# Kernel tuning notes

Measured on AMD Instinct MI355X. Metric: run time of the kernel, lower is better.

## Reference

```python
import jax, jax.numpy as jnp
import numpy as np

N_NODES = 50000
N_EDGES = 200000
N_GRAPH = 1024
H = 128          # hidden_channels
POS = 48         # pos_offset
NF = 256         # num_filters in SchNetInteraction
L = 5            # n_layers
NFF = 512
MAX_ITEM = 300


def ssp(v):
    # shifted softplus used by SchNet
    return jax.nn.softplus(v) - jnp.log(2.0)


def setup_inputs() -> dict:
    key = jax.random.key(0)
    ks = iter(jax.random.split(key, 40))
    s = 0.05
    inp = {}
    inp['x'] = jax.random.randint(next(ks), (N_NODES,), 0, MAX_ITEM)
    inp['edge_index'] = jax.random.randint(next(ks), (2, N_EDGES), 0, N_NODES)
    inp['edge_attr'] = jax.random.normal(next(ks), (N_EDGES, 4), jnp.float32)
    inp['batch'] = jnp.sort(jax.random.randint(next(ks), (N_NODES,), 0, N_GRAPH))
    inp['pos'] = jax.random.normal(next(ks), (N_NODES, 3), jnp.float32)
    # embedding / projection params
    vert = jax.random.normal(next(ks), (MAX_ITEM + 1, H - POS), jnp.float32) * s
    inp['vert_emb'] = vert.at[MAX_ITEM].set(0.0)  # padding_idx
    inp['pos_w'] = jax.random.normal(next(ks), (POS, 3), jnp.float32) * s
    inp['edge_w'] = jax.random.normal(next(ks), (H, 4), jnp.float32) * s
    # per-layer SchNetInteraction params (stacked over L)
    inp['filt_w1'] = jax.random.normal(next(ks), (L, NF, H), jnp.float32) * s
    inp['filt_b1'] = jnp.zeros((L, NF), jnp.float32)
    inp['filt_w2'] = jax.random.normal(next(ks), (L, NF, NF), jnp.float32) * s
    inp['filt_b2'] = jnp.zeros((L, NF), jnp.float32)
    inp['lin1_w'] = jax.random.normal(next(ks), (L, NF, H), jnp.float32) * s
    inp['lin2_w'] = jax.random.normal(next(ks), (L, H, NF), jnp.float32) * s
    inp['lin2_b'] = jnp.zeros((L, H), jnp.float32)
    inp['lin3_w'] = jax.random.normal(next(ks), (L, H, H), jnp.float32) * s
    inp['lin3_b'] = jnp.zeros((L, H), jnp.float32)
    # per-layer edge MLP: Linear(edge_ch + in_ch -> in_ch) + Tanh
    inp['em_w'] = jax.random.normal(next(ks), (L, H, 2 * H), jnp.float32) * s
    inp['em_b'] = jnp.zeros((L, H), jnp.float32)
    # head
    inp['head_w1'] = jax.random.normal(next(ks), (NFF, H), jnp.float32) * s
    inp['head_b1'] = jnp.zeros((NFF,), jnp.float32)
    inp['head_w2'] = jax.random.normal(next(ks), (1, NFF), jnp.float32) * s
    inp['head_b2'] = jnp.zeros((1,), jnp.float32)
    return inp


def _forward(x, edge_index, edge_attr, batch, pos, vert_emb, pos_w, edge_w,
             filt_w1, filt_b1, filt_w2, filt_b2, lin1_w, lin2_w, lin2_b,
             lin3_w, lin3_b, em_w, em_b, head_w1, head_b1, head_w2, head_b2):
    n = x.shape[0]
    src, dst = edge_index[0], edge_index[1]
    h = jnp.concatenate([vert_emb[x], pos @ pos_w.T], axis=-1)  # [N, H]
    ea = edge_attr @ edge_w.T                                    # [E, H]
    for i in range(L):
        # SchNetInteraction / CFConv: per-edge filter MLP, gather, scatter-sum
        W = ssp(ea @ filt_w1[i].T + filt_b1[i]) @ filt_w2[i].T + filt_b2[i]  # [E, NF]
        hj = (h @ lin1_w[i].T)[src]                                          # [E, NF]
        agg = jax.ops.segment_sum(hj * W, dst, num_segments=n)               # [N, NF]
        out = ssp(agg @ lin2_w[i].T + lin2_b[i]) @ lin3_w[i].T + lin3_b[i]   # [N, H]
        h = jax.nn.relu(out) + h  # relu + residual skip
        # edge MLP update (always active in ResGraphModule)
        ea = jnp.tanh(jnp.concatenate([ea, h[src] + h[dst]], axis=-1) @ em_w[i].T + em_b[i]) + ea
    # global mean pool over graphs
    ssum = jax.ops.segment_sum(h, batch, num_segments=N_GRAPH)               # [G, H]
    cnt = jax.ops.segment_sum(jnp.ones((n,), h.dtype), batch, num_segments=N_GRAPH)
    g = ssum / jnp.maximum(cnt, 1.0)[:, None]
    # head: Linear -> GELU (exact, as torch default) -> Dropout(eval) -> Linear
    y = jax.nn.gelu(g @ head_w1.T + head_b1, approximate=False) @ head_w2.T + head_b2
    return y  # [G, 1]


def reference(x, edge_index, edge_attr, batch, pos, vert_emb, pos_w, edge_w,
              filt_w1, filt_b1, filt_w2, filt_b2, lin1_w, lin2_w, lin2_b,
              lin3_w, lin3_b, em_w, em_b, head_w1, head_b1, head_w2, head_b2):
    return _forward(x, edge_index, edge_attr, batch, pos, vert_emb, pos_w, edge_w,
                    filt_w1, filt_b1, filt_w2, filt_b2, lin1_w, lin2_w, lin2_b,
                    lin3_w, lin3_b, em_w, em_b, head_w1, head_b1, head_w2, head_b2)
```

## Files before the change

### kernel.cpp

```cpp
#include <hip/hip_runtime.h>
#include <hip/hip_bf16.h>
#include <math.h>

#define N_NODES 50000
#define N_EDGES 200000
#define N_GRAPH 1024
#define HC      128
#define NFC     256
#define NLAYER  5
#define NFFC    512

typedef short bf16x8 __attribute__((ext_vector_type(8)));
typedef float f4v    __attribute__((ext_vector_type(4)));

__device__ __forceinline__ float ssp_f(float x) {
  float e = __expf(-fabsf(x));
  return fmaxf(x, 0.0f) + __logf(1.0f + e) - 0.69314718055994530942f;
}
__device__ __forceinline__ float tanh_f(float x) {
  float e = __expf(2.0f * fabsf(x));
  float t = 1.0f - 2.0f * __builtin_amdgcn_rcpf(e + 1.0f);
  return copysignf(t, x);
}
__device__ __forceinline__ unsigned short f2bf(float x) {
  union { float f; unsigned u; } v; v.f = x;
  unsigned r = v.u + 0x7fff + ((v.u >> 16) & 1);
  return (unsigned short)(r >> 16);
}
__device__ __forceinline__ float bf2f(unsigned short b) {
  union { unsigned u; float f; } v; v.u = (unsigned)b << 16; return v.f;
}

__device__ __forceinline__ int swzA(int row, int col) {
  return (row << 7) + (((col >> 3) ^ (row & 7)) << 3) + (col & 7);
}
__device__ __forceinline__ int swzT(int row, int col) {
  return (row << 8) + (((col >> 3) ^ (row & 7)) << 3) + (col & 7);
}

__global__ void zero_kernel(float4* __restrict__ p, int n4) {
  int i = blockIdx.x * blockDim.x + threadIdx.x;
  if (i < n4) p[i] = make_float4(0.f, 0.f, 0.f, 0.f);
}
__global__ void zeroi_kernel(int* __restrict__ p, int n) {
  int i = blockIdx.x * blockDim.x + threadIdx.x;
  if (i < n) p[i] = 0;
}

__global__ void hist_kernel(const int* __restrict__ ei, int* __restrict__ deg) {
  int e = blockIdx.x * blockDim.x + threadIdx.x;
  if (e < N_EDGES) atomicAdd(&deg[ei[N_EDGES + e]], 1);
}
__global__ void scan1_kernel(const int* __restrict__ deg, int* __restrict__ excl,
                             int* __restrict__ bsum, int n) {
  __shared__ int buf[256];
  const int tid = threadIdx.x;
  const int i = blockIdx.x * 256 + tid;
  int v = (i < n) ? deg[i] : 0;
  buf[tid] = v;
  __syncthreads();
  for (int s = 1; s < 256; s <<= 1) {
    int t = (tid >= s) ? buf[tid - s] : 0;
    __syncthreads();
    buf[tid] += t;
    __syncthreads();
  }
  if (i < n) excl[i] = buf[tid] - v;
  if (tid == 255) bsum[blockIdx.x] = buf[255];
}
__global__ void scan2_kernel(int* __restrict__ bsum, int nb) {
  __shared__ int buf[256];
  const int tid = threadIdx.x;
  int v = (tid < nb) ? bsum[tid] : 0;
  buf[tid] = v;
  __syncthreads();
  for (int s = 1; s < 256; s <<= 1) {
    int t = (tid >= s) ? buf[tid - s] : 0;
    __syncthreads();
    buf[tid] += t;
    __syncthreads();
  }
  if (tid < nb) bsum[tid] = buf[tid] - v;
}
__global__ void scan3_kernel(int* __restrict__ excl, const int* __restrict__ bsum, int n) {
  int i = blockIdx.x * 256 + threadIdx.x;
  if (i < n) excl[i] += bsum[blockIdx.x];
}
__global__ void perm_kernel(const int* __restrict__ ei, int* __restrict__ cursor,
                            int* __restrict__ perm) {
  int e = blockIdx.x * blockDim.x + threadIdx.x;
  if (e < N_EDGES) {
    int d = ei[N_EDGES + e];
    int p = atomicAdd(&cursor[d], 1);
    perm[p] = e;
  }
}
__global__ void eperm_kernel(const int* __restrict__ ei, const int* __restrict__ perm,
                             int* __restrict__ eiPs, int* __restrict__ eiPd,
                             int* __restrict__ ipos) {
  int p = blockIdx.x * blockDim.x + threadIdx.x;
  if (p < N_EDGES) {
    int e = perm[p];
    eiPs[p] = ei[e];
    eiPd[p] = ei[N_EDGES + e];
    ipos[e] = p;
  }
}

__global__ void wconv_kernel(const float* __restrict__ w,
                             unsigned short* __restrict__ hi, int n) {
  int i = blockIdx.x * blockDim.x + threadIdx.x;
  if (i < n) hi[i] = f2bf(w[i]);
}

__global__ void embed_kernel(const int* __restrict__ x, const float* __restrict__ pos,
                             const float* __restrict__ vert, const float* __restrict__ posw,
                             unsigned short* __restrict__ h) {
  int n = blockIdx.x;
  int c = threadIdx.x;
  float v;
  if (c < 80) {
    v = vert[(size_t)x[n] * 80 + c];
  } else {
    int j = c - 80;
    v = pos[n*3+0]*posw[j*3+0] + pos[n*3+1]*posw[j*3+1] + pos[n*3+2]*posw[j*3+2];
  }
  h[(size_t)n*HC + c] = f2bf(v);
}

__global__ void edgeproj_kernel(const float* __restrict__ eattr, const float* __restrict__ ew,
                                unsigned short* __restrict__ eaP,
                                const int* __restrict__ ipos) {
  int idx = blockIdx.x * blockDim.x + threadIdx.x;
  if (idx >= N_EDGES * HC) return;
  int e = idx >> 7, c = idx & 127;
  const float* a = eattr + (size_t)e*4;
  const float* w = ew + (size_t)c*4;
  eaP[(size_t)ipos[e]*HC + c] = f2bf(a[0]*w[0] + a[1]*w[1] + a[2]*w[2] + a[3]*w[3]);
}

__global__ __launch_bounds__(256, 4) void emlite_kernel(
    unsigned short* eaP,
    const unsigned short* __restrict__ Bh,
    const float* __restrict__ bias,
    const int* __restrict__ eiPs, const int* __restrict__ eiPd,
    const unsigned short* __restrict__ hfeat)
{
  __shared__ unsigned short ldsA[64 * 128];
  __shared__ unsigned short ldsH[64 * 128];

  const int tid  = threadIdx.x;
  const int m0   = blockIdx.x * 64;
  const int lane = tid & 63, wave = tid >> 6;
  const int quad = lane >> 4, l16 = lane & 15;
  const int r = tid >> 2, cb = (tid & 3) * 32;

  const int e = m0 + r;
  const int s = eiPs[e], d = eiPd[e];

  {
    const unsigned short* ap = eaP + (size_t)e * HC + cb;
#pragma unroll
    for (int q = 0; q < 4; q++)
      *(bf16x8*)&ldsA[swzA(r, cb + q*8)] = *(const bf16x8*)(ap + q*8);
    const unsigned short* p1 = hfeat + (size_t)s * HC + cb;
    const unsigned short* p2 = hfeat + (size_t)d * HC + cb;
    unsigned short x1[32], x2[32], th[32];
#pragma unroll
    for (int q = 0; q < 4; q++) {
      *(bf16x8*)&x1[q*8] = *(const bf16x8*)(p1 + q*8);
      *(bf16x8*)&x2[q*8] = *(const bf16x8*)(p2 + q*8);
    }
#pragma unroll
    for (int j = 0; j < 32; j++) th[j] = f2bf(bf2f(x1[j]) + bf2f(x2[j]));
#pragma unroll
    for (int q = 0; q < 4; q++)
      *(bf16x8*)&ldsH[swzA(r, cb + q*8)] = *(bf16x8*)&th[q*8];
  }

  const f4v zf = {0.f, 0.f, 0.f, 0.f};
  f4v acc[4][2];
#pragma unroll
  for (int mt = 0; mt < 4; mt++) { acc[mt][0] = zf; acc[mt][1] = zf; }

  bf16x8 bn = *(const bf16x8*)&Bh[(size_t)(wave*32 + l16) * 2*HC + quad*8];

  __syncthreads();

#pragma unroll
  for (int g = 0; g < 16; g++) {
    const int nt = g >> 3, hf = (g >> 2) & 1, ki = g & 3;
    bf16x8 bc = bn;
    if (g < 15) {
      const int g1 = g + 1;
      const int nt1 = g1 >> 3, hf1 = (g1 >> 2) & 1, ki1 = g1 & 3;
      bn = *(const bf16x8*)&Bh[(size_t)(wave*32 + nt1*16 + l16) * 2*HC
                               + hf1*HC + ki1*32 + quad*8];
    }
    const unsigned short* src = hf ? ldsH : ldsA;
#pragma unroll
    for (int mt = 0; mt < 4; mt++) {
      bf16x8 a = *(const bf16x8*)&src[swzA(mt*16 + l16, ki*32 + quad*8)];
      acc[mt][nt] = __builtin_amdgcn_mfma_f32_16x16x32_bf16(a, bc, acc[mt][nt], 0, 0, 0);
    }
  }

#pragma unroll
  for (int nt = 0; nt < 2; nt++) {
    const int col = wave*32 + nt*16 + l16;
    const float bz = bias[col];
#pragma unroll
    for (int mt = 0; mt < 4; mt++) {
      const int rowb = mt*16 + quad*4;
#pragma unroll
      for (int rr = 0; rr < 4; rr++) {
        const size_t idx = (size_t)(m0 + rowb + rr) * HC + col;
        eaP[idx] = f2bf(tanh_f(acc[mt][nt][rr] + bz) + bf2f(ldsA[swzA(rowb + rr, col)]));
      }
    }
  }
}

__global__ __launch_bounds__(256, 4) void nodeup_kernel(
    float* __restrict__ agg,
    const unsigned short* __restrict__ L2h,
    const float* __restrict__ b2,
    const unsigned short* __restrict__ L3h,
    const float* __restrict__ b3,
    unsigned short* h)
{
  __shared__ unsigned short ldsS[64 * 256];

  const int tid  = threadIdx.x;
  const int m0   = blockIdx.x * 64;
  const int lane = tid & 63, wave = tid >> 6;
  const int quad = lane >> 4, l16 = lane & 15;
  const int wn = wave * 32;
  const int r  = tid >> 2;
  const int cb2 = (tid & 3) * 64;

  const bool mok = (m0 + r) < N_NODES;

  if (mok) {
    const float* ap = agg + (size_t)(m0 + r) * NFC + cb2;
#pragma unroll
    for (int g = 0; g < 8; g++) {
      float4 v0 = *(const float4*)(ap + g*8);
      float4 v1 = *(const float4*)(ap + g*8 + 4);
      unsigned short th[8];
      th[0] = f2bf(v0.x); th[1] = f2bf(v0.y); th[2] = f2bf(v0.z); th[3] = f2bf(v0.w);
      th[4] = f2bf(v1.x); th[5] = f2bf(v1.y); th[6] = f2bf(v1.z); th[7] = f2bf(v1.w);
      *(bf16x8*)&ldsS[swzT(r, cb2 + g*8)] = *(bf16x8*)th;
    }
    float4* zp = (float4*)(agg + (size_t)(m0 + r) * NFC + cb2);
    const float4 z4 = make_float4(0.f, 0.f, 0.f, 0.f);
#pragma unroll
    for (int g = 0; g < 16; g++) zp[g] = z4;
  } else {
    const bf16x8 zb = {0, 0, 0, 0, 0, 0, 0, 0};
#pragma unroll
    for (int g = 0; g < 8; g++) *(bf16x8*)&ldsS[swzT(r, cb2 + g*8)] = zb;
  }

  const f4v zf = {0.f, 0.f, 0.f, 0.f};
  f4v acc[4][2];
#pragma unroll
  for (int i = 0; i < 4; i++) { acc[i][0] = zf; acc[i][1] = zf; }

  bf16x8 bn[2];
#pragma unroll
  for (int nt = 0; nt < 2; nt++)
    bn[nt] = *(const bf16x8*)&L2h[(size_t)(wn + nt*16 + l16) * NFC + quad*8];

  __syncthreads();

  for (int kki = 0; kki < 8; kki++) {
    bf16x8 bc[2] = {bn[0], bn[1]};
    if (kki < 7) {
#pragma unroll
      for (int nt = 0; nt < 2; nt++)
        bn[nt] = *(const bf16x8*)&L2h[(size_t)(wn + nt*16 + l16) * NFC
                                      + (kki+1)*32 + quad*8];
    }
    bf16x8 a[4];
#pragma unroll
    for (int t = 0; t < 4; t++)
      a[t] = *(const bf16x8*)&ldsS[swzT(t*16 + l16, kki*32 + quad*8)];
#pragma unroll
    for (int mt = 0; mt < 4; mt++)
#pragma unroll
      for (int nt = 0; nt < 2; nt++)
        acc[mt][nt] = __builtin_amdgcn_mfma_f32_16x16x32_bf16(a[mt], bc[nt], acc[mt][nt], 0, 0, 0);
  }
  __syncthreads();

#pragma unroll
  for (int nt = 0; nt < 2; nt++) {
    const int col = wn + nt*16 + l16;
    const float bz = b2[col];
#pragma unroll
    for (int mt = 0; mt < 4; mt++) {
      const int rowb = mt*16 + quad*4;
#pragma unroll
      for (int rr = 0; rr < 4; rr++)
        ldsS[swzA(rowb+rr, col)] = f2bf(ssp_f(acc[mt][nt][rr] + bz));
    }
  }

  bf16x8 b3n[2];
#pragma unroll
  for (int nt = 0; nt < 2; nt++)
    b3n[nt] = *(const bf16x8*)&L3h[(size_t)(wn + nt*16 + l16) * HC + quad*8];

  __syncthreads();

  f4v acc2[4][2];
#pragma unroll
  for (int i = 0; i < 4; i++) { acc2[i][0] = zf; acc2[i][1] = zf; }

  for (int kki = 0; kki < 4; kki++) {
    bf16x8 bc[2] = {b3n[0], b3n[1]};
    if (kki < 3) {
#pragma unroll
      for (int nt = 0; nt < 2; nt++)
        b3n[nt] = *(const bf16x8*)&L3h[(size_t)(wn + nt*16 + l16) * HC
                                       + (kki+1)*32 + quad*8];
    }
    bf16x8 a[4];
#pragma unroll
    for (int t = 0; t < 4; t++)
      a[t] = *(const bf16x8*)&ldsS[swzA(t*16 + l16, kki*32 + quad*8)];
#pragma unroll
    for (int mt = 0; mt < 4; mt++)
#pragma unroll
      for (int nt = 0; nt < 2; nt++)
        acc2[mt][nt] = __builtin_amdgcn_mfma_f32_16x16x32_bf16(a[mt], bc[nt], acc2[mt][nt], 0, 0, 0);
  }

#pragma unroll
  for (int nt = 0; nt < 2; nt++) {
    const int ncol = wn + nt*16 + l16;
    const float bz = b3[ncol];
#pragma unroll
    for (int mt = 0; mt < 4; mt++) {
      const int mb = mt*16 + quad*4;
#pragma unroll
      for (int rr = 0; rr < 4; rr++) {
        const int m = m0 + mb + rr;
        if (m < N_NODES) {
          const size_t idx = (size_t)m * HC + ncol;
          h[idx] = f2bf(fmaxf(acc2[mt][nt][rr] + bz, 0.f) + bf2f(h[idx]));
        }
      }
    }
  }
}

__device__ __forceinline__ int sigma_row(int r) {
  return ((r >> 2) & 3) * 16 + (r >> 4) * 4 + (r & 3);
}
__global__ __launch_bounds__(256, 3) void ffs_kernel(
    const unsigned short* __restrict__ eaP,
    const unsigned short* __restrict__ l1h,
    const unsigned short* __restrict__ fw1h,
    const float* __restrict__ fb1,
    const unsigned short* __restrict__ fw2h,
    const float* __restrict__ fb2,
    const int* __restrict__ eiPs, const int* __restrict__ eiPd,
    const unsigned short* __restrict__ hfeat, float* __restrict__ agg)
{
  __shared__ unsigned short ldsA[64 * 128];
  __shared__ unsigned short ldsT[64 * 256];
  __shared__ int sD[64];

  const int tid  = threadIdx.x;
  const int m0   = blockIdx.x * 64;
  const int lane = tid & 63, wave = tid >> 6;
  const int quad = lane >> 4, l16 = lane & 15;
  const int r = tid >> 2, cb = (tid & 3) * 32;
  const int sp = m0 + sigma_row(r);

  const int s = eiPs[sp];
  bf16x8 hreg[4];
  {
    const unsigned short* hp = hfeat + (size_t)s * HC + cb;
#pragma unroll
    for (int q = 0; q < 4; q++) hreg[q] = *(const bf16x8*)(hp + q*8);
  }
  if (tid < 64) sD[tid] = eiPd[m0 + sigma_row(tid)];

  {
    const unsigned short* ap = eaP + (size_t)sp * HC + cb;
#pragma unroll
    for (int q = 0; q < 4; q++)
      *(bf16x8*)&ldsA[swzA(r, cb + q*8)] = *(const bf16x8*)(ap + q*8);
  }

  const f4v zf = {0.f, 0.f, 0.f, 0.f};
  __syncthreads();

  for (int p = 0; p < 4; p++) {
    f4v tacc[4];
#pragma unroll
    for (int mt = 0; mt < 4; mt++) tacc[mt] = zf;
    const size_t b1row = (size_t)(p*64 + wave*16 + l16);
#pragma unroll
    for (int kk = 0; kk < 128; kk += 32) {
      bf16x8 b = *(const bf16x8*)&fw1h[b1row * HC + kk + quad*8];
#pragma unroll
      for (int mt = 0; mt < 4; mt++) {
        bf16x8 a = *(const bf16x8*)&ldsA[swzA(mt*16 + l16, kk + quad*8)];
        tacc[mt] = __builtin_amdgcn_mfma_f32_16x16x32_bf16(a, b, tacc[mt], 0, 0, 0);
      }
    }
    const int col = p*64 + wave*16 + l16;
    const float bz = fb1[col];
#pragma unroll
    for (int mt = 0; mt < 4; mt++) {
      const int rowb = mt*16 + quad*4;
#pragma unroll
      for (int rr = 0; rr < 4; rr++)
        ldsT[swzT(rowb+rr, col)] = f2bf(ssp_f(tacc[mt][rr] + bz));
    }
  }
  __syncthreads();

#pragma unroll
  for (int q = 0; q < 4; q++)
    *(bf16x8*)&ldsA[swzA(r, cb + q*8)] = hreg[q];

  f4v wacc[4][4];
#pragma unroll
  for (int mt = 0; mt < 4; mt++)
#pragma unroll
    for (int nt = 0; nt < 4; nt++) wacc[mt][nt] = zf;

  __builtin_amdgcn_s_setprio(1);
  for (int p = 0; p < 4; p++) {
#pragma unroll
    for (int kc = 0; kc < 2; kc++) {
      bf16x8 a_[4];
#pragma unroll
      for (int mt = 0; mt < 4; mt++)
        a_[mt] = *(const bf16x8*)&ldsT[swzT(mt*16 + l16, p*64 + kc*32 + quad*8)];
#pragma unroll
      for (int nt = 0; nt < 4; nt++) {
        const size_t brow = (size_t)(wave*64 + nt*16 + l16);
        bf16x8 b = *(const bf16x8*)&fw2h[brow * NFC + p*64 + kc*32 + quad*8];
#pragma unroll
        for (int mt = 0; mt < 4; mt++)
          wacc[mt][nt] = __builtin_amdgcn_mfma_f32_16x16x32_bf16(a_[mt], b, wacc[mt][nt], 0, 0, 0);
      }
    }
  }
  __builtin_amdgcn_s_setprio(0);
  __syncthreads();

  f4v hacc[4][4];
#pragma unroll
  for (int mt = 0; mt < 4; mt++)
#pragma unroll
    for (int nt = 0; nt < 4; nt++) hacc[mt][nt] = zf;

#pragma unroll
  for (int kk = 0; kk < 128; kk += 32) {
    bf16x8 a_[4];
#pragma unroll
    for (int mt = 0; mt < 4; mt++)
      a_[mt] = *(const bf16x8*)&ldsA[swzA(mt*16 + l16, kk + quad*8)];
#pragma unroll
    for (int nt = 0; nt < 4; nt++) {
      const size_t brow = (size_t)(wave*64 + nt*16 + l16);
      bf16x8 b = *(const bf16x8*)&l1h[brow * HC + kk + quad*8];
#pragma unroll
      for (int mt = 0; mt < 4; mt++)
        hacc[mt][nt] = __builtin_amdgcn_mfma_f32_16x16x32_bf16(a_[mt], b, hacc[mt][nt], 0, 0, 0);
    }
  }

#pragma unroll
  for (int nt = 0; nt < 4; nt++) {
    const int col = wave*64 + nt*16 + l16;
    const float bz = fb2[col];
    float accum = 0.f;
    int prev = -1;
    bool firstrun = true;
#pragma unroll
    for (int mt = 0; mt < 4; mt++) {
#pragma unroll
      for (int rr = 0; rr < 4; rr++) {
        const int prow = mt*16 + quad*4 + rr;
        const int d = sD[prow];
        const float v = (wacc[mt][nt][rr] + bz) * hacc[mt][nt][rr];
        if (d != prev) {
          if (prev >= 0) {
            if (firstrun) atomicAdd(&agg[(size_t)prev * NFC + col], accum);
            else          agg[(size_t)prev * NFC + col] = accum;
            firstrun = false;
          }
          accum = v; prev = d;
        } else {
          accum += v;
        }
      }
    }
    atomicAdd(&agg[(size_t)prev * NFC + col], accum);
  }
}

__global__ __launch_bounds__(256) void poolhead_kernel(
    const int* __restrict__ batch, const unsigned short* __restrict__ h,
    const float* __restrict__ w1, const float* __restrict__ b1,
    const float* __restrict__ w2, const float* __restrict__ b2,
    float* __restrict__ y)
{
  __shared__ float gs[HC];
  __shared__ float red[256];
  const int g = blockIdx.x;
  const int tid = threadIdx.x;

  int lo = 0, hi = N_NODES;
  while (lo < hi) { int m = (lo + hi) >> 1; if (batch[m] < g) lo = m + 1; else hi = m; }
  int lo2 = lo, hi2 = N_NODES;
  while (lo2 < hi2) { int m = (lo2 + hi2) >> 1; if (batch[m] < g + 1) lo2 = m + 1; else hi2 = m; }
  const int cnt = lo2 - lo;

  if (tid < HC) {
    float s = 0.f;
    for (int i = lo; i < lo2; i++) s += bf2f(h[(size_t)i * HC + tid]);
    gs[tid] = s / (float)max(cnt, 1);
  }
  __syncthreads();

  float partial = 0.f;
  for (int f = tid; f < NFFC; f += 256) {
    float acc = b1[f];
    const float* wr = w1 + (size_t)f * HC;
#pragma unroll 8
    for (int k = 0; k < HC; k++) acc = fmaf(gs[k], wr[k], acc);
    float t = 0.5f * acc * (1.0f + erff(acc * 0.70710678118654752440f));
    partial = fmaf(t, w2[f], partial);
  }
  red[tid] = partial;
  __syncthreads();
  for (int s = 128; s > 0; s >>= 1) {
    if (tid < s) red[tid] += red[tid + s];
    __syncthreads();
  }
  if (tid == 0) y[g] = red[0] + b2[0];
}

extern "C" void kernel_launch(void* const* d_in, const int* in_sizes, int n_in,
                              void* d_out, int out_size, void* d_ws, size_t ws_size,
                              hipStream_t stream) {
  const int*   x     = (const int*)  d_in[0];
  const int*   ei    = (const int*)  d_in[1];
  const float* eattr = (const float*)d_in[2];
  const int*   batch = (const int*)  d_in[3];
  const float* pos   = (const float*)d_in[4];
  const float* vert  = (const float*)d_in[5];
  const float* posw  = (const float*)d_in[6];
  const float* edgew = (const float*)d_in[7];
  const float* fw1   = (const float*)d_in[8];
  const float* fb1   = (const float*)d_in[9];
  const float* fw2   = (const float*)d_in[10];
  const float* fb2   = (const float*)d_in[11];
  const float* l1w   = (const float*)d_in[12];
  const float* l2w   = (const float*)d_in[13];
  const float* l2b   = (const float*)d_in[14];
  const float* l3w   = (const float*)d_in[15];
  const float* l3b   = (const float*)d_in[16];
  const float* emw   = (const float*)d_in[17];
  const float* emb   = (const float*)d_in[18];
  const float* hw1   = (const float*)d_in[19];
  const float* hb1   = (const float*)d_in[20];
  const float* hw2   = (const float*)d_in[21];
  const float* hb2   = (const float*)d_in[22];
  float* out = (float*)d_out;

  char* ws = (char*)d_ws;
  size_t off = 0;
  auto alloc = [&](size_t bytes) { char* p = ws + off; off += (bytes + 511) & ~(size_t)511; return p; };
  unsigned short* eaP = (unsigned short*)alloc((size_t)N_EDGES*HC*2);
  unsigned short* h   = (unsigned short*)alloc((size_t)N_NODES*HC*2);
  float* agg  = (float*)alloc((size_t)N_NODES*NFC*4);
  int* deg    = (int*)alloc((size_t)(N_NODES+1)*4);
  int* cursor = (int*)alloc((size_t)(N_NODES+1)*4);
  int* bsum   = (int*)alloc((size_t)256*4);
  int* perm   = (int*)alloc((size_t)N_EDGES*4);
  int* eiPs   = (int*)alloc((size_t)N_EDGES*4);
  int* eiPd   = (int*)alloc((size_t)N_EDGES*4);
  int* ipos   = (int*)alloc((size_t)N_EDGES*4);
  const int n_fw1 = NLAYER*NFC*HC, n_fw2 = NLAYER*NFC*NFC, n_l1 = NLAYER*NFC*HC;
  const int n_l2 = NLAYER*HC*NFC, n_l3 = NLAYER*HC*HC, n_em = NLAYER*HC*2*HC;
  unsigned short* fw1h = (unsigned short*)alloc((size_t)n_fw1*2);
  unsigned short* fw2h = (unsigned short*)alloc((size_t)n_fw2*2);
  unsigned short* l1h  = (unsigned short*)alloc((size_t)n_l1*2);
  unsigned short* l2h  = (unsigned short*)alloc((size_t)n_l2*2);
  unsigned short* l3h  = (unsigned short*)alloc((size_t)n_l3*2);
  unsigned short* emh  = (unsigned short*)alloc((size_t)n_em*2);

  const int NSCAN = N_NODES + 1;
  const int NB    = (NSCAN + 255) / 256;

  zeroi_kernel<<<(NSCAN+255)/256, 256, 0, stream>>>(deg, NSCAN);
  hist_kernel<<<(N_EDGES+255)/256, 256, 0, stream>>>(ei, deg);
  scan1_kernel<<<NB, 256, 0, stream>>>(deg, cursor, bsum, NSCAN);
  scan2_kernel<<<1, 256, 0, stream>>>(bsum, NB);
  scan3_kernel<<<NB, 256, 0, stream>>>(cursor, bsum, NSCAN);
  perm_kernel<<<(N_EDGES+255)/256, 256, 0, stream>>>(ei, cursor, perm);
  eperm_kernel<<<(N_EDGES+255)/256, 256, 0, stream>>>(ei, perm, eiPs, eiPd, ipos);

  wconv_kernel<<<(n_fw1+255)/256, 256, 0, stream>>>(fw1, fw1h, n_fw1);
  wconv_kernel<<<(n_fw2+255)/256, 256, 0, stream>>>(fw2, fw2h, n_fw2);
  wconv_kernel<<<(n_l1 +255)/256, 256, 0, stream>>>(l1w, l1h, n_l1);
  wconv_kernel<<<(n_l2 +255)/256, 256, 0, stream>>>(l2w, l2h, n_l2);
  wconv_kernel<<<(n_l3 +255)/256, 256, 0, stream>>>(l3w, l3h, n_l3);
  wconv_kernel<<<(n_em +255)/256, 256, 0, stream>>>(emw, emh, n_em);

  const int GN   = (N_NODES + 63) / 64;
  const int GE64 = N_EDGES / 64;

  embed_kernel<<<N_NODES, 128, 0, stream>>>(x, pos, vert, posw, h);
  edgeproj_kernel<<<(N_EDGES*HC + 255)/256, 256, 0, stream>>>(eattr, edgew, eaP, ipos);
  zero_kernel<<<((N_NODES*NFC/4) + 255)/256, 256, 0, stream>>>(
      (float4*)agg, N_NODES*NFC/4);

  for (int i = 0; i < NLAYER; ++i) {
    ffs_kernel<<<GE64, 256, 0, stream>>>(
        eaP, l1h + (size_t)i*NFC*HC,
        fw1h + (size_t)i*NFC*HC, fb1 + (size_t)i*NFC,
        fw2h + (size_t)i*NFC*NFC, fb2 + (size_t)i*NFC,
        eiPs, eiPd, h, agg);
    nodeup_kernel<<<GN, 256, 0, stream>>>(
        agg, l2h + (size_t)i*HC*NFC, l2b + (size_t)i*HC,
        l3h + (size_t)i*HC*HC, l3b + (size_t)i*HC, h);
    if (i < NLAYER - 1) {
      emlite_kernel<<<GE64, 256, 0, stream>>>(
          eaP, emh + (size_t)i*HC*2*HC, emb + (size_t)i*HC,
          eiPs, eiPd, h);
    }
  }

  poolhead_kernel<<<N_GRAPH, 256, 0, stream>>>(batch, h, hw1, hb1, hw2, hb2, out);
}
```

Before: 1.458 ms.

## Split filter GEMM into halves to shrink LDS and raise ffs occupancy

Restructures ffs_kernel so the ssp filter intermediate is produced and consumed in two 128-column halves. This halves the ldsT buffer, and the launch bound is raised to 4 blocks per CU. The h-feature gather is deferred into the second half, and the lin1 GEMM plus scatter epilogue is split into two column halves to cut live accumulators. Block indices are also remapped by XCD so consecutive edge tiles land on the same XCD. The cost is extra barriers and the risk of register spills under the tighter launch bound.

```diff
diff --git a/kernel.cpp b/kernel.cpp
--- a/kernel.cpp
+++ b/kernel.cpp
@@ -359,7 +359,7 @@
 __device__ __forceinline__ int sigma_row(int r) {
   return ((r >> 2) & 3) * 16 + (r >> 4) * 4 + (r & 3);
 }
-__global__ __launch_bounds__(256, 3) void ffs_kernel(
+__global__ __launch_bounds__(256, 4) void ffs_kernel(
     const unsigned short* __restrict__ eaP,
     const unsigned short* __restrict__ l1h,
     const unsigned short* __restrict__ fw1h,
@@ -370,23 +370,20 @@
     const unsigned short* __restrict__ hfeat, float* __restrict__ agg)
 {
   __shared__ unsigned short ldsA[64 * 128];
-  __shared__ unsigned short ldsT[64 * 256];
+  __shared__ unsigned short ldsTh[64 * 128];
   __shared__ int sD[64];
 
   const int tid  = threadIdx.x;
-  const int m0   = blockIdx.x * 64;
+  const int bid = blockIdx.x;
+  const int xcd = bid & 7, bi = bid >> 3;
+  const int wg  = (xcd < 5) ? xcd * 391 + bi : 5 * 391 + (xcd - 5) * 390 + bi;
+  const int m0   = wg * 64;
   const int lane = tid & 63, wave = tid >> 6;
   const int quad = lane >> 4, l16 = lane & 15;
   const int r = tid >> 2, cb = (tid & 3) * 32;
   const int sp = m0 + sigma_row(r);
 
   const int s = eiPs[sp];
-  bf16x8 hreg[4];
-  {
-    const unsigned short* hp = hfeat + (size_t)s * HC + cb;
-#pragma unroll
-    for (int q = 0; q < 4; q++) hreg[q] = *(const bf16x8*)(hp + q*8);
-  }
   if (tid < 64) sD[tid] = eiPd[m0 + sigma_row(tid)];
 
   {
@@ -397,37 +394,7 @@
   }
 
   const f4v zf = {0.f, 0.f, 0.f, 0.f};
-  __syncthreads();
-
-  for (int p = 0; p < 4; p++) {
-    f4v tacc[4];
-#pragma unroll
-    for (int mt = 0; mt < 4; mt++) tacc[mt] = zf;
-    const size_t b1row = (size_t)(p*64 + wave*16 + l16);
-#pragma unroll
-    for (int kk = 0; kk < 128; kk += 32) {
-      bf16x8 b = *(const bf16x8*)&fw1h[b1row * HC + kk + quad*8];
-#pragma unroll
-      for (int mt = 0; mt < 4; mt++) {
-        bf16x8 a = *(const bf16x8*)&ldsA[swzA(mt*16 + l16, kk + quad*8)];
-        tacc[mt] = __builtin_amdgcn_mfma_f32_16x16x32_bf16(a, b, tacc[mt], 0, 0, 0);
-      }
-    }
-    const int col = p*64 + wave*16 + l16;
-    const float bz = fb1[col];
-#pragma unroll
-    for (int mt = 0; mt < 4; mt++) {
-      const int rowb = mt*16 + quad*4;
-#pragma unroll
-      for (int rr = 0; rr < 4; rr++)
-        ldsT[swzT(rowb+rr, col)] = f2bf(ssp_f(tacc[mt][rr] + bz));
-    }
-  }
-  __syncthreads();
-
-#pragma unroll
-  for (int q = 0; q < 4; q++)
-    *(bf16x8*)&ldsA[swzA(r, cb + q*8)] = hreg[q];
+  const int bcol = wave*16 + l16;
 
   f4v wacc[4][4];
 #pragma unroll
@@ -435,76 +402,127 @@
 #pragma unroll
     for (int nt = 0; nt < 4; nt++) wacc[mt][nt] = zf;
 
-  __builtin_amdgcn_s_setprio(1);
-  for (int p = 0; p < 4; p++) {
-#pragma unroll
-    for (int kc = 0; kc < 2; kc++) {
-      bf16x8 a_[4];
-#pragma unroll
-      for (int mt = 0; mt < 4; mt++)
-        a_[mt] = *(const bf16x8*)&ldsT[swzT(mt*16 + l16, p*64 + kc*32 + quad*8)];
-#pragma unroll
-      for (int nt = 0; nt < 4; nt++) {
-        const size_t brow = (size_t)(wave*64 + nt*16 + l16);
-        bf16x8 b = *(const bf16x8*)&fw2h[brow * NFC + p*64 + kc*32 + quad*8];
-#pragma unroll
-        for (int mt = 0; mt < 4; mt++)
-          wacc[mt][nt] = __builtin_amdgcn_mfma_f32_16x16x32_bf16(a_[mt], b, wacc[mt][nt], 0, 0, 0);
-      }
-    }
-  }
-  __builtin_amdgcn_s_setprio(0);
-  __syncthreads();
-
-  f4v hacc[4][4];
-#pragma unroll
-  for (int mt = 0; mt < 4; mt++)
-#pragma unroll
-    for (int nt = 0; nt < 4; nt++) hacc[mt][nt] = zf;
-
-#pragma unroll
-  for (int kk = 0; kk < 128; kk += 32) {
-    bf16x8 a_[4];
-#pragma unroll
-    for (int mt = 0; mt < 4; mt++)
-      a_[mt] = *(const bf16x8*)&ldsA[swzA(mt*16 + l16, kk + quad*8)];
-#pragma unroll
-    for (int nt = 0; nt < 4; nt++) {
-      const size_t brow = (size_t)(wave*64 + nt*16 + l16);
-      bf16x8 b = *(const bf16x8*)&l1h[brow * HC + kk + quad*8];
-#pragma unroll
-      for (int mt = 0; mt < 4; mt++)
-        hacc[mt][nt] = __builtin_amdgcn_mfma_f32_16x16x32_bf16(a_[mt], b, hacc[mt][nt], 0, 0, 0);
-    }
-  }
-
-#pragma unroll
-  for (int nt = 0; nt < 4; nt++) {
-    const int col = wave*64 + nt*16 + l16;
-    const float bz = fb2[col];
-    float accum = 0.f;
-    int prev = -1;
-    bool firstrun = true;
-#pragma unroll
-    for (int mt = 0; mt < 4; mt++) {
-#pragma unroll
-      for (int rr = 0; rr < 4; rr++) {
-        const int prow = mt*16 + quad*4 + rr;
-        const int d = sD[prow];
-        const float v = (wacc[mt][nt][rr] + bz) * hacc[mt][nt][rr];
-        if (d != prev) {
-          if (prev >= 0) {
-            if (firstrun) atomicAdd(&agg[(size_t)prev * NFC + col], accum);
-            else          agg[(size_t)prev * NFC + col] = accum;
-            firstrun = false;
-          }
-          accum = v; prev = d;
-        } else {
-          accum += v;
+  __syncthreads();
+
+  for (int half = 0; half < 2; half++) {
+#pragma unroll
+    for (int p2 = 0; p2 < 2; p2++) {
+      const int p = half*2 + p2;
+      f4v tacc[4];
+#pragma unroll
+      for (int mt = 0; mt < 4; mt++) tacc[mt] = zf;
+      const size_t b1row = (size_t)(p*64 + bcol);
+#pragma unroll
+      for (int kk = 0; kk < 128; kk += 32) {
+        bf16x8 b = *(const bf16x8*)&fw1h[b1row * HC + kk + quad*8];
+#pragma unroll
+        for (int mt = 0; mt < 4; mt++) {
+          bf16x8 a = *(const bf16x8*)&ldsA[swzA(mt*16 + l16, kk + quad*8)];
+          tacc[mt] = __builtin_amdgcn_mfma_f32_16x16x32_bf16(a, b, tacc[mt], 0, 0, 0);
         }
       }
-    }
-    atomicAdd(&agg[(size_t)prev * NFC + col], accum);
+      const int colh = p2*64 + bcol;
+      const float bz = fb1[p*64 + bcol];
+#pragma unroll
+      for (int mt = 0; mt < 4; mt++) {
+        const int rowb = mt*16 + quad*4;
+#pragma unroll
+        for (int rr = 0; rr < 4; rr++)
+          ldsTh[swzA(rowb+rr, colh)] = f2bf(ssp_f(tacc[mt][rr] + bz));
+      }
+    }
+    __syncthreads();
+
+    bf16x8 hreg0, hreg1, hreg2, hreg3;
+    if (half == 1) {
+      const unsigned short* hp = hfeat + (size_t)s * HC + cb;
+      hreg0 = *(const bf16x8*)(hp);
+      hreg1 = *(const bf16x8*)(hp + 8);
+      hreg2 = *(const bf16x8*)(hp + 16);
+      hreg3 = *(const bf16x8*)(hp + 24);
+    }
+
+    __builtin_amdgcn_s_setprio(1);
+#pragma unroll
+    for (int p2 = 0; p2 < 2; p2++) {
+      const int p = half*2 + p2;
+#pragma unroll
+      for (int kc = 0; kc < 2; kc++) {
+        bf16x8 a_[4];
+#pragma unroll
+        for (int mt = 0; mt < 4; mt++)
+          a_[mt] = *(const bf16x8*)&ldsTh[swzA(mt*16 + l16, p2*64 + kc*32 + quad*8)];
+#pragma unroll
+        for (int nt = 0; nt < 4; nt++) {
+          const size_t brow = (size_t)(wave*64 + nt*16 + l16);
+          bf16x8 b = *(const bf16x8*)&fw2h[brow * NFC + p*64 + kc*32 + quad*8];
+#pragma unroll
+          for (int mt = 0; mt < 4; mt++)
+            wacc[mt][nt] = __builtin_amdgcn_mfma_f32_16x16x32_bf16(a_[mt], b, wacc[mt][nt], 0, 0, 0);
+        }
+      }
+    }
+    __builtin_amdgcn_s_setprio(0);
+
+    if (half == 1) {
+      *(bf16x8*)&ldsA[swzA(r, cb)]      = hreg0;
+      *(bf16x8*)&ldsA[swzA(r, cb + 8)]  = hreg1;
+      *(bf16x8*)&ldsA[swzA(r, cb + 16)] = hreg2;
+      *(bf16x8*)&ldsA[swzA(r, cb + 24)] = hreg3;
+    }
+    __syncthreads();
+  }
+
+#pragma unroll
+  for (int hf = 0; hf < 2; hf++) {
+    f4v hacc[4][2];
+#pragma unroll
+    for (int mt = 0; mt < 4; mt++) { hacc[mt][0] = zf; hacc[mt][1] = zf; }
+
+#pragma unroll
+    for (int kk = 0; kk < 128; kk += 32) {
+      bf16x8 a_[4];
+#pragma unroll
+      for (int mt = 0; mt < 4; mt++)
+        a_[mt] = *(const bf16x8*)&ldsA[swzA(mt*16 + l16, kk + quad*8)];
+#pragma unroll
+      for (int nt = 0; nt < 2; nt++) {
+        const size_t brow = (size_t)(wave*64 + (hf*2 + nt)*16 + l16);
+        bf16x8 b = *(const bf16x8*)&l1h[brow * HC + kk + quad*8];
+#pragma unroll
+        for (int mt = 0; mt < 4; mt++)
+          hacc[mt][nt] = __builtin_amdgcn_mfma_f32_16x16x32_bf16(a_[mt], b, hacc[mt][nt], 0, 0, 0);
+      }
+    }
+
+#pragma unroll
+    for (int nt = 0; nt < 2; nt++) {
+      const int col = wave*64 + (hf*2 + nt)*16 + l16;
+      const float bz = fb2[col];
+      float accum = 0.f;
+      int prev = -1;
+      bool firstrun = true;
+#pragma unroll
+      for (int mt = 0; mt < 4; mt++) {
+#pragma unroll
+        for (int rr = 0; rr < 4; rr++) {
+          const int prow = mt*16 + quad*4 + rr;
+          const int d = sD[prow];
+          const float v = (wacc[mt][hf*2 + nt][rr] + bz) * hacc[mt][nt][rr];
+          if (d != prev) {
+            if (prev >= 0) {
+              if (firstrun) atomicAdd(&agg[(size_t)prev * NFC + col], accum);
+              else          agg[(size_t)prev * NFC + col] = accum;
+              firstrun = false;
+            }
+            accum = v; prev = d;
+          } else {
+            accum += v;
+          }
+        }
+      }
+      atomicAdd(&agg[(size_t)prev * NFC + col], accum);
+    }
   }
 }
 
```

Result: slower. 1.894 ms (+29.9%).

## Fuse edge-MLP update into next layer's filter/scatter kernel

Applied to the files above, without the earlier changes.

Removes the separate emlite kernel and performs the edge-MLP update (tanh(concat(ea, h_src+h_dst) W + b) + ea) at the start of the next layer's ffs kernel, keeping the updated edge features in LDS for the filter GEMM. This saves one launch per layer and a full read-write of the edge feature tensor plus a reread of the h source rows. The updated edges are still written back to global memory for the following layer. It reuses ldsT as scratch for h sums and adds register pressure to a kernel already bounded at three blocks per CU.

```diff
diff --git a/kernel.cpp b/kernel.cpp
--- a/kernel.cpp
+++ b/kernel.cpp
@@ -139,88 +139,6 @@
   eaP[(size_t)ipos[e]*HC + c] = f2bf(a[0]*w[0] + a[1]*w[1] + a[2]*w[2] + a[3]*w[3]);
 }
 
-__global__ __launch_bounds__(256, 4) void emlite_kernel(
-    unsigned short* eaP,
-    const unsigned short* __restrict__ Bh,
-    const float* __restrict__ bias,
-    const int* __restrict__ eiPs, const int* __restrict__ eiPd,
-    const unsigned short* __restrict__ hfeat)
-{
-  __shared__ unsigned short ldsA[64 * 128];
-  __shared__ unsigned short ldsH[64 * 128];
-
-  const int tid  = threadIdx.x;
-  const int m0   = blockIdx.x * 64;
-  const int lane = tid & 63, wave = tid >> 6;
-  const int quad = lane >> 4, l16 = lane & 15;
-  const int r = tid >> 2, cb = (tid & 3) * 32;
-
-  const int e = m0 + r;
-  const int s = eiPs[e], d = eiPd[e];
-
-  {
-    const unsigned short* ap = eaP + (size_t)e * HC + cb;
-#pragma unroll
-    for (int q = 0; q < 4; q++)
-      *(bf16x8*)&ldsA[swzA(r, cb + q*8)] = *(const bf16x8*)(ap + q*8);
-    const unsigned short* p1 = hfeat + (size_t)s * HC + cb;
-    const unsigned short* p2 = hfeat + (size_t)d * HC + cb;
-    unsigned short x1[32], x2[32], th[32];
-#pragma unroll
-    for (int q = 0; q < 4; q++) {
-      *(bf16x8*)&x1[q*8] = *(const bf16x8*)(p1 + q*8);
-      *(bf16x8*)&x2[q*8] = *(const bf16x8*)(p2 + q*8);
-    }
-#pragma unroll
-    for (int j = 0; j < 32; j++) th[j] = f2bf(bf2f(x1[j]) + bf2f(x2[j]));
-#pragma unroll
-    for (int q = 0; q < 4; q++)
-      *(bf16x8*)&ldsH[swzA(r, cb + q*8)] = *(bf16x8*)&th[q*8];
-  }
-
-  const f4v zf = {0.f, 0.f, 0.f, 0.f};
-  f4v acc[4][2];
-#pragma unroll
-  for (int mt = 0; mt < 4; mt++) { acc[mt][0] = zf; acc[mt][1] = zf; }
-
-  bf16x8 bn = *(const bf16x8*)&Bh[(size_t)(wave*32 + l16) * 2*HC + quad*8];
-
-  __syncthreads();
-
-#pragma unroll
-  for (int g = 0; g < 16; g++) {
-    const int nt = g >> 3, hf = (g >> 2) & 1, ki = g & 3;
-    bf16x8 bc = bn;
-    if (g < 15) {
-      const int g1 = g + 1;
-      const int nt1 = g1 >> 3, hf1 = (g1 >> 2) & 1, ki1 = g1 & 3;
-      bn = *(const bf16x8*)&Bh[(size_t)(wave*32 + nt1*16 + l16) * 2*HC
-                               + hf1*HC + ki1*32 + quad*8];
-    }
-    const unsigned short* src = hf ? ldsH : ldsA;
-#pragma unroll
-    for (int mt = 0; mt < 4; mt++) {
-      bf16x8 a = *(const bf16x8*)&src[swzA(mt*16 + l16, ki*32 + quad*8)];
-      acc[mt][nt] = __builtin_amdgcn_mfma_f32_16x16x32_bf16(a, bc, acc[mt][nt], 0, 0, 0);
-    }
-  }
-
-#pragma unroll
-  for (int nt = 0; nt < 2; nt++) {
-    const int col = wave*32 + nt*16 + l16;
-    const float bz = bias[col];
-#pragma unroll
-    for (int mt = 0; mt < 4; mt++) {
-      const int rowb = mt*16 + quad*4;
-#pragma unroll
-      for (int rr = 0; rr < 4; rr++) {
-        const size_t idx = (size_t)(m0 + rowb + rr) * HC + col;
-        eaP[idx] = f2bf(tanh_f(acc[mt][nt][rr] + bz) + bf2f(ldsA[swzA(rowb + rr, col)]));
-      }
-    }
-  }
-}
-
 __global__ __launch_bounds__(256, 4) void nodeup_kernel(
     float* __restrict__ agg,
     const unsigned short* __restrict__ L2h,
@@ -359,19 +277,20 @@
 __device__ __forceinline__ int sigma_row(int r) {
   return ((r >> 2) & 3) * 16 + (r >> 4) * 4 + (r & 3);
 }
-__global__ __launch_bounds__(256, 3) void ffs_kernel(
-    const unsigned short* __restrict__ eaP,
+__global__ __launch_bounds__(256, 3) void emffs_kernel(
+    unsigned short* eaP,
+    const unsigned short* __restrict__ emWh, const float* __restrict__ emB,
     const unsigned short* __restrict__ l1h,
-    const unsigned short* __restrict__ fw1h,
-    const float* __restrict__ fb1,
-    const unsigned short* __restrict__ fw2h,
-    const float* __restrict__ fb2,
+    const unsigned short* __restrict__ fw1h, const float* __restrict__ fb1,
+    const unsigned short* __restrict__ fw2h, const float* __restrict__ fb2,
     const int* __restrict__ eiPs, const int* __restrict__ eiPd,
-    const unsigned short* __restrict__ hfeat, float* __restrict__ agg)
+    const unsigned short* __restrict__ hfeat, float* __restrict__ agg,
+    const int do_em)
 {
   __shared__ unsigned short ldsA[64 * 128];
   __shared__ unsigned short ldsT[64 * 256];
   __shared__ int sD[64];
+  unsigned short* ldsH = ldsT;
 
   const int tid  = threadIdx.x;
   const int m0   = blockIdx.x * 64;
@@ -396,8 +315,77 @@
       *(bf16x8*)&ldsA[swzA(r, cb + q*8)] = *(const bf16x8*)(ap + q*8);
   }
 
+  if (do_em) {
+    const int d = eiPd[sp];
+    const unsigned short* dp = hfeat + (size_t)d * HC + cb;
+    unsigned short th[32];
+#pragma unroll
+    for (int q = 0; q < 4; q++) {
+      bf16x8 x2 = *(const bf16x8*)(dp + q*8);
+#pragma unroll
+      for (int j = 0; j < 8; j++) {
+        unsigned short a16 = ((const unsigned short*)&hreg[q])[j];
+        unsigned short b16 = ((const unsigned short*)&x2)[j];
+        th[q*8 + j] = f2bf(bf2f(a16) + bf2f(b16));
+      }
+    }
+#pragma unroll
+    for (int q = 0; q < 4; q++)
+      *(bf16x8*)&ldsH[swzA(r, cb + q*8)] = *(bf16x8*)&th[q*8];
+  }
+
   const f4v zf = {0.f, 0.f, 0.f, 0.f};
-  __syncthreads();
+
+  bf16x8 bn;
+  if (do_em)
+    bn = *(const bf16x8*)&emWh[(size_t)(wave*32 + l16) * 2*HC + quad*8];
+
+  __syncthreads();
+
+  if (do_em) {
+    f4v eacc[4][2];
+#pragma unroll
+    for (int mt = 0; mt < 4; mt++) { eacc[mt][0] = zf; eacc[mt][1] = zf; }
+#pragma unroll
+    for (int g = 0; g < 16; g++) {
+      const int nt = g >> 3, hf = (g >> 2) & 1, ki = g & 3;
+      bf16x8 bc = bn;
+      if (g < 15) {
+        const int g1 = g + 1;
+        const int nt1 = g1 >> 3, hf1 = (g1 >> 2) & 1, ki1 = g1 & 3;
+        bn = *(const bf16x8*)&emWh[(size_t)(wave*32 + nt1*16 + l16) * 2*HC
+                                   + hf1*HC + ki1*32 + quad*8];
+      }
+      const unsigned short* src = hf ? ldsH : ldsA;
+#pragma unroll
+      for (int mt = 0; mt < 4; mt++) {
+        bf16x8 a = *(const bf16x8*)&src[swzA(mt*16 + l16, ki*32 + quad*8)];
+        eacc[mt][nt] = __builtin_amdgcn_mfma_f32_16x16x32_bf16(a, bc, eacc[mt][nt], 0, 0, 0);
+      }
+    }
+#pragma unroll
+    for (int nt = 0; nt < 2; nt++) {
+      const int col = wave*32 + nt*16 + l16;
+      const float bz = emB[col];
+#pragma unroll
+      for (int mt = 0; mt < 4; mt++) {
+        const int rowb = mt*16 + quad*4;
+#pragma unroll
+        for (int rr = 0; rr < 4; rr++) {
+          const int row = rowb + rr;
+          ldsA[swzA(row, col)] = f2bf(tanh_f(eacc[mt][nt][rr] + bz)
+                                      + bf2f(ldsA[swzA(row, col)]));
+        }
+      }
+    }
+    __syncthreads();
+    {
+      unsigned short* op = eaP + (size_t)sp * HC + cb;
+#pragma unroll
+      for (int q = 0; q < 4; q++)
+        *(bf16x8*)(op + q*8) = *(const bf16x8*)&ldsA[swzA(r, cb + q*8)];
+    }
+  }
 
   for (int p = 0; p < 4; p++) {
     f4v tacc[4];
@@ -627,19 +615,17 @@
       (float4*)agg, N_NODES*NFC/4);
 
   for (int i = 0; i < NLAYER; ++i) {
-    ffs_kernel<<<GE64, 256, 0, stream>>>(
-        eaP, l1h + (size_t)i*NFC*HC,
+    const int em_i = (i > 0) ? (i - 1) : 0;
+    emffs_kernel<<<GE64, 256, 0, stream>>>(
+        eaP,
+        emh + (size_t)em_i*HC*2*HC, emb + (size_t)em_i*HC,
+        l1h + (size_t)i*NFC*HC,
         fw1h + (size_t)i*NFC*HC, fb1 + (size_t)i*NFC,
         fw2h + (size_t)i*NFC*NFC, fb2 + (size_t)i*NFC,
-        eiPs, eiPd, h, agg);
+        eiPs, eiPd, h, agg, (i > 0) ? 1 : 0);
     nodeup_kernel<<<GN, 256, 0, stream>>>(
         agg, l2h + (size_t)i*HC*NFC, l2b + (size_t)i*HC,
         l3h + (size_t)i*HC*HC, l3b + (size_t)i*HC, h);
-    if (i < NLAYER - 1) {
-      emlite_kernel<<<GE64, 256, 0, stream>>>(
-          eaP, emh + (size_t)i*HC*2*HC, emb + (size_t)i*HC,
-          eiPs, eiPd, h);
-    }
   }
 
   poolhead_kernel<<<N_GRAPH, 256, 0, stream>>>(batch, h, hw1, hb1, hw2, hb2, out);
```

Result: faster. 1.412 ms (-3.1%).
